# Optimization experiments

Measured on AMD Instinct MI355X. Metric: run time of the kernel, lower is better.

The kernel has to match this reference:

```python
import jax, jax.numpy as jnp
import numpy as np

N_NODES = 100000
N_EDGES = 1600000
D = 128
EPS = 0.0  # train_eps=False -> constant


def setup_inputs() -> dict:
    key = jax.random.key(0)
    k = jax.random.split(key, 6)
    s = 1.0 / np.sqrt(D)
    return {
        "X": jax.random.normal(k[0], (N_NODES, D), dtype=jnp.float32),
        "W1": jax.random.normal(k[1], (D, D), dtype=jnp.float32) * s,
        "b1": jnp.zeros((D,), dtype=jnp.float32),
        "W2": jax.random.normal(k[2], (D, D), dtype=jnp.float32) * s,
        "b2": jnp.zeros((D,), dtype=jnp.float32),
        "edge_src": jax.random.randint(k[3], (N_EDGES,), 0, N_NODES, dtype=jnp.int32),
        "edge_dst": jax.random.randint(k[4], (N_EDGES,), 0, N_NODES, dtype=jnp.int32),
    }


def reference(X, W1, b1, W2, b2, edge_src, edge_dst):
    # v2v sum aggregation: agg[i] = sum_{j in N(i)} X[j]
    msgs = X[edge_src]  # (E, D) gather
    agg = jax.ops.segment_sum(msgs, edge_dst, num_segments=N_NODES)  # (N, D)
    h = (1.0 + EPS) * X + agg
    # MLP: Linear -> ReLU -> Linear
    h = jax.nn.relu(h @ W1 + b1)
    out = h @ W2 + b2
    return out
```

## Files before the change

### kernel.cpp

```cpp
#include <hip/hip_runtime.h>
#include <hip/hip_bf16.h>

#define N_NODES 100000
#define N_EDGES 1600000
#define D 128

#define BINSHIFT 8
#define NB2 391
#define EPB 8192
#define RBLK 196
#define EBUF_CAP 4864

#define HEAD_W_BLOCKS 8
#define HEAD_CVT_BLOCKS 3125

#define PADK 136

typedef __bf16 bf16x8 __attribute__((ext_vector_type(8)));
typedef short short8 __attribute__((ext_vector_type(8)));
typedef float f32x4 __attribute__((ext_vector_type(4)));

__device__ __forceinline__ unsigned short f2bf(float f) {
  union { float f; unsigned u; } c; c.f = f;
  unsigned u = c.u;
  u += 0x7FFFu + ((u >> 16) & 1u);
  return (unsigned short)(u >> 16);
}
__device__ __forceinline__ float bflo(unsigned u) {
  union { unsigned u; float f; } c; c.u = u << 16; return c.f;
}
__device__ __forceinline__ float bfhi(unsigned u) {
  union { unsigned u; float f; } c; c.u = u & 0xFFFF0000u; return c.f;
}

__launch_bounds__(512)
__global__ void k_head(const int* __restrict__ esrc, const int* __restrict__ edst,
                       unsigned* __restrict__ binbuf, int* __restrict__ cntmatT,
                       int* __restrict__ startmatT,
                       const float* __restrict__ X, unsigned short* __restrict__ Xb,
                       const float* __restrict__ W1, const float* __restrict__ W2,
                       unsigned short* __restrict__ Wimg) {
  const int b = blockIdx.x, t = threadIdx.x;

  if (b < RBLK) {
    __shared__ unsigned lbuf[EPB];
    __shared__ int cnt[NB2];
    __shared__ int base[NB2];
    __shared__ int cur[NB2];
    __shared__ int scanb[512];
    const int e0 = b * EPB;
    const int ne = min(EPB, N_EDGES - e0);

    for (int i = t; i < NB2; i += 512) { cnt[i] = 0; cur[i] = 0; }
    __syncthreads();
    for (int i = t; i < ne; i += 512)
      atomicAdd(&cnt[edst[e0 + i] >> BINSHIFT], 1);
    __syncthreads();
    scanb[t] = (t < NB2) ? cnt[t] : 0;
    __syncthreads();
    for (int d = 1; d < 512; d <<= 1) {
      int x = (t >= d) ? scanb[t - d] : 0;
      __syncthreads();
      scanb[t] += x;
      __syncthreads();
    }
    if (t < NB2) base[t] = scanb[t] - cnt[t];
    __syncthreads();
    for (int i = t; i < ne; i += 512) {
      int d = edst[e0 + i];
      int s = esrc[e0 + i];
      int bi = d >> BINSHIFT;
      int pos = base[bi] + atomicAdd(&cur[bi], 1);
      lbuf[pos] = ((unsigned)(d & 255) << 17) | (unsigned)s;
    }
    __syncthreads();
    uint4* dst4 = (uint4*)(binbuf + (size_t)b * EPB);
    const uint4* src4 = (const uint4*)lbuf;
    for (int i = t; i < EPB / 4; i += 512) dst4[i] = src4[i];
    if (t < NB2) {
      cntmatT[t * RBLK + b] = cnt[t];
      startmatT[t * RBLK + b] = base[t];
    }
    return;
  }
  if (b < RBLK + HEAD_W_BLOCKS) {
    int bb = b - RBLK;
    const float* W = (bb & 4) ? W2 : W1;
    unsigned short* img = Wimg + ((bb & 4) ? 128 * PADK : 0);
    int k0 = (bb & 3) * 32;
#pragma unroll
    for (int it = 0; it < 8; ++it) {
      int idx = it * 512 + t;
      int k = k0 + (idx >> 7), n = idx & 127;
      img[n * PADK + k] = f2bf(W[k * 128 + n]);
    }
    return;
  }
  size_t i = ((size_t)(b - RBLK - HEAD_W_BLOCKS) * 512 + t) * 8;
  const float4* p = (const float4*)(X + i);
  float4 a = p[0], c = p[1];
  short8 s;
  s[0] = f2bf(a.x); s[1] = f2bf(a.y); s[2] = f2bf(a.z); s[3] = f2bf(a.w);
  s[4] = f2bf(c.x); s[5] = f2bf(c.y); s[6] = f2bf(c.z); s[7] = f2bf(c.w);
  *(short8*)(Xb + i) = s;
}

__launch_bounds__(1024)
__global__ void k_sortgather(const unsigned* __restrict__ binbuf,
                             const int* __restrict__ cntmatT,
                             const int* __restrict__ startmatT,
                             const unsigned* __restrict__ X1,
                             unsigned* __restrict__ h0) {
  __shared__ unsigned ebuf[EBUF_CAP];
  __shared__ unsigned ebuf2[EBUF_CAP];
  __shared__ int hist[256];
  __shared__ int scn[256];
  __shared__ int nstart[256];
  __shared__ int ncnt[256];
  __shared__ int rcnt[RBLK];
  __shared__ int roff[RBLK];
  __shared__ int eoff[RBLK];
  __shared__ int s_total;

  const int b = blockIdx.x, t = threadIdx.x;
  const int n0 = b << BINSHIFT;
  const int wv = t >> 6, ln = t & 63;

  if (t < RBLK) {
    rcnt[t] = cntmatT[b * RBLK + t];
    roff[t] = startmatT[b * RBLK + t];
  }
  __syncthreads();

  if (t < 256) scn[t] = (t < RBLK) ? rcnt[t] : 0;
  __syncthreads();
  for (int d = 1; d < 256; d <<= 1) {
    int x = 0;
    if (t < 256 && t >= d) x = scn[t - d];
    __syncthreads();
    if (t < 256) scn[t] += x;
    __syncthreads();
  }
  if (t < RBLK) eoff[t] = scn[t] - rcnt[t];
  if (t == RBLK - 1) s_total = scn[t];
  __syncthreads();
  const int mytotal = s_total;

  for (int r = wv; r < RBLK; r += 16) {
    const unsigned* src = binbuf + (size_t)r * EPB + roff[r];
    int c = rcnt[r], o = eoff[r];
    for (int i = ln; i < c; i += 64) ebuf[o + i] = src[i];
  }
  if (t < 256) hist[t] = 0;
  __syncthreads();

  for (int i = t; i < mytotal; i += 1024)
    atomicAdd(&hist[ebuf[i] >> 17], 1);
  __syncthreads();
  int v = (t < 256) ? hist[t] : 0;
  if (t < 256) scn[t] = v;
  __syncthreads();
  for (int d = 1; d < 256; d <<= 1) {
    int x = 0;
    if (t < 256 && t >= d) x = scn[t - d];
    __syncthreads();
    if (t < 256) scn[t] += x;
    __syncthreads();
  }
  if (t < 256) {
    nstart[t] = scn[t] - v;
    ncnt[t] = v;
    hist[t] = scn[t] - v;
  }
  __syncthreads();
  for (int i = t; i < mytotal; i += 1024) {
    unsigned e = ebuf[i];
    int pos = atomicAdd(&hist[e >> 17], 1);
    ebuf2[pos] = e & 0x1FFFFu;
  }
  __syncthreads();

  for (int j = 0; j < 16; ++j) {
    int li = wv * 16 + j;
    int node = n0 + li;
    if (node >= N_NODES) break;
    unsigned u = X1[(size_t)node * 64 + ln];
    float hx = bflo(u), hy = bfhi(u);
    int e = nstart[li];
    int end = e + ncnt[li];
    for (; e + 8 <= end; e += 8) {
      int s0 = ebuf2[e],     s1 = ebuf2[e + 1], s2 = ebuf2[e + 2], s3 = ebuf2[e + 3];
      int s4 = ebuf2[e + 4], s5 = ebuf2[e + 5], s6 = ebuf2[e + 6], s7 = ebuf2[e + 7];
      unsigned u0 = X1[(size_t)s0 * 64 + ln];
      unsigned u1 = X1[(size_t)s1 * 64 + ln];
      unsigned u2 = X1[(size_t)s2 * 64 + ln];
      unsigned u3 = X1[(size_t)s3 * 64 + ln];
      unsigned u4 = X1[(size_t)s4 * 64 + ln];
      unsigned u5 = X1[(size_t)s5 * 64 + ln];
      unsigned u6 = X1[(size_t)s6 * 64 + ln];
      unsigned u7 = X1[(size_t)s7 * 64 + ln];
      hx += bflo(u0); hy += bfhi(u0);
      hx += bflo(u1); hy += bfhi(u1);
      hx += bflo(u2); hy += bfhi(u2);
      hx += bflo(u3); hy += bfhi(u3);
      hx += bflo(u4); hy += bfhi(u4);
      hx += bflo(u5); hy += bfhi(u5);
      hx += bflo(u6); hy += bfhi(u6);
      hx += bflo(u7); hy += bfhi(u7);
    }
    for (; e + 2 <= end; e += 2) {
      unsigned u0 = X1[(size_t)ebuf2[e] * 64 + ln];
      unsigned u1 = X1[(size_t)ebuf2[e + 1] * 64 + ln];
      hx += bflo(u0); hy += bfhi(u0);
      hx += bflo(u1); hy += bfhi(u1);
    }
    for (; e < end; ++e) {
      unsigned u0 = X1[(size_t)ebuf2[e] * 64 + ln];
      hx += bflo(u0); hy += bfhi(u0);
    }
    h0[(size_t)node * 64 + ln] = ((unsigned)f2bf(hy) << 16) | f2bf(hx);
  }
}

#define BR2 128

__launch_bounds__(512, 4)
__global__ void k_mlp2(const unsigned short* __restrict__ h0,
                       const unsigned short* __restrict__ Wimg,
                       const float* __restrict__ b1v, const float* __restrict__ b2v,
                       float* __restrict__ out) {
  __shared__ __attribute__((aligned(16))) unsigned short lW[128 * PADK];
  __shared__ __attribute__((aligned(16))) unsigned short lH[BR2 * PADK];

  const int t = threadIdx.x;
  const int wave = t >> 6, lane = t & 63;
  const int lr = lane & 15, lg = lane >> 4;
  const int row0 = blockIdx.x * BR2;
  const int wrow = row0 + wave * 16;

  const uint4* wi = (const uint4*)Wimg;
  uint4* lw = (uint4*)lW;

  for (int i = t; i < 2176; i += 512) lw[i] = wi[i];

  bf16x8 a[4];
#pragma unroll
  for (int kb = 0; kb < 4; ++kb) {
    int r = wrow + lr;
    if (r >= N_NODES) r = N_NODES - 1;
    a[kb] = __builtin_bit_cast(bf16x8,
        *(const short8*)(h0 + (size_t)r * D + kb * 32 + lg * 8));
  }

  f32x4 acc[8];
#pragma unroll
  for (int nc = 0; nc < 8; ++nc) {
    float bb = b1v[nc * 16 + lr];
    acc[nc] = (f32x4){bb, bb, bb, bb};
  }

  __syncthreads();

#pragma unroll
  for (int nc = 0; nc < 8; ++nc) {
#pragma unroll
    for (int kb = 0; kb < 4; ++kb) {
      bf16x8 b = *(const bf16x8*)&lW[(nc * 16 + lr) * PADK + kb * 32 + lg * 8];
      acc[nc] = __builtin_amdgcn_mfma_f32_16x16x32_bf16(a[kb], b, acc[nc], 0, 0, 0);
    }
  }

  __syncthreads();

  {
    const uint4* wi2 = (const uint4*)Wimg + 2176;
    for (int i = t; i < 2176; i += 512) lw[i] = wi2[i];
  }

#pragma unroll
  for (int nc = 0; nc < 8; ++nc) {
#pragma unroll
    for (int r = 0; r < 4; ++r) {
      float v = acc[nc][r];
      v = v > 0.f ? v : 0.f;
      lH[(wave * 16 + lg * 4 + r) * PADK + nc * 16 + lr] = f2bf(v);
    }
  }

  __syncthreads();

  bf16x8 a2[4];
#pragma unroll
  for (int kb = 0; kb < 4; ++kb)
    a2[kb] = *(const bf16x8*)&lH[(wave * 16 + lr) * PADK + kb * 32 + lg * 8];

#pragma unroll
  for (int nc = 0; nc < 8; ++nc) {
    float bb = b2v[nc * 16 + lr];
    acc[nc] = (f32x4){bb, bb, bb, bb};
  }

#pragma unroll
  for (int nc = 0; nc < 8; ++nc) {
#pragma unroll
    for (int kb = 0; kb < 4; ++kb) {
      bf16x8 b = *(const bf16x8*)&lW[(nc * 16 + lr) * PADK + kb * 32 + lg * 8];
      acc[nc] = __builtin_amdgcn_mfma_f32_16x16x32_bf16(a2[kb], b, acc[nc], 0, 0, 0);
    }
  }

#pragma unroll
  for (int nc = 0; nc < 8; ++nc) {
#pragma unroll
    for (int r = 0; r < 4; ++r) {
      int row = wrow + lg * 4 + r;
      if (row < N_NODES) out[(size_t)row * D + nc * 16 + lr] = acc[nc][r];
    }
  }
}


__global__ void k_hist(const int* __restrict__ dst, int* __restrict__ deg) {
  int i = blockIdx.x * 256 + threadIdx.x;
  if (i < N_EDGES) atomicAdd(&deg[dst[i]], 1);
}

__global__ void k_scan1(const int* __restrict__ deg, int* __restrict__ offs,
                        int* __restrict__ bsum) {
  __shared__ int s[1024];
  int t = threadIdx.x;
  int i = blockIdx.x * 1024 + t;
  int v = (i < N_NODES) ? deg[i] : 0;
  s[t] = v;
  __syncthreads();
  for (int d = 1; d < 1024; d <<= 1) {
    int x = (t >= d) ? s[t - d] : 0;
    __syncthreads();
    s[t] += x;
    __syncthreads();
  }
  if (i < N_NODES) offs[i] = s[t] - v;
  if (t == 1023) bsum[blockIdx.x] = s[t];
}

__global__ void k_scan2(int* __restrict__ bsum) {
  __shared__ int s[128];
  int t = threadIdx.x;
  int v = (t < 98) ? bsum[t] : 0;
  s[t] = v;
  __syncthreads();
  for (int d = 1; d < 128; d <<= 1) {
    int x = (t >= d) ? s[t - d] : 0;
    __syncthreads();
    s[t] += x;
    __syncthreads();
  }
  if (t < 98) bsum[t] = s[t] - v;
}

__global__ void k_scan3(int* __restrict__ offs, const int* __restrict__ bsum) {
  int i = blockIdx.x * 1024 + threadIdx.x;
  if (i < N_NODES) offs[i] += bsum[blockIdx.x];
}

__global__ void k_bucket(const int* __restrict__ src, const int* __restrict__ dst,
                         int* __restrict__ offs, int* __restrict__ srt) {
  int i = blockIdx.x * 256 + threadIdx.x;
  if (i < N_EDGES) {
    int pos = atomicAdd(&offs[dst[i]], 1);
    srt[pos] = src[i];
  }
}

__global__ void k_gather(const float* __restrict__ X, const int* __restrict__ deg,
                         const int* __restrict__ offs, const int* __restrict__ srt,
                         float* __restrict__ out) {
  int node = blockIdx.x * 4 + (threadIdx.x >> 6);
  int lane = threadIdx.x & 63;
  const float2* X2 = (const float2*)X;
  float2 h = X2[(size_t)node * 64 + lane];
  int end = offs[node];
  int dg = deg[node];
  for (int e = end - dg; e < end; ++e) {
    int s = srt[e];
    float2 x = X2[(size_t)s * 64 + lane];
    h.x += x.x; h.y += x.y;
  }
  ((float2*)out)[(size_t)node * 64 + lane] = h;
}

#define BR 256

__launch_bounds__(512, 1)
__global__ void k_mlp(const float* __restrict__ h0,
                      const float* __restrict__ W1, const float* __restrict__ b1,
                      const float* __restrict__ W2, const float* __restrict__ b2,
                      float* __restrict__ out) {
  __shared__ __attribute__((aligned(16))) unsigned short lW[2 * 128 * PADK];
  __shared__ __attribute__((aligned(16))) unsigned short lH[BR * PADK];

  const int t = threadIdx.x;
  const int wave = t >> 6, lane = t & 63;
  const int lr = lane & 15, lg = lane >> 4;
  const int row0 = blockIdx.x * BR;
  const int wrow = row0 + wave * 32;

  for (int i = t; i < 128 * 128; i += 512) {
    int k = i >> 7, n = i & 127;
    lW[n * PADK + k] = f2bf(W1[i]);
    lW[128 * PADK + n * PADK + k] = f2bf(W2[i]);
  }

  bf16x8 a[2][4];
#pragma unroll
  for (int tr = 0; tr < 2; ++tr) {
#pragma unroll
    for (int kb = 0; kb < 4; ++kb) {
      int r = wrow + tr * 16 + lr;
      if (r >= N_NODES) r = N_NODES - 1;
      const float4* p = (const float4*)(h0 + (size_t)r * D + kb * 32 + lg * 8);
      float4 f0 = p[0], f1 = p[1];
      short8 s;
      s[0] = f2bf(f0.x); s[1] = f2bf(f0.y); s[2] = f2bf(f0.z); s[3] = f2bf(f0.w);
      s[4] = f2bf(f1.x); s[5] = f2bf(f1.y); s[6] = f2bf(f1.z); s[7] = f2bf(f1.w);
      a[tr][kb] = __builtin_bit_cast(bf16x8, s);
    }
  }

  f32x4 acc[2][8];
#pragma unroll
  for (int nc = 0; nc < 8; ++nc) {
    float bb = b1[nc * 16 + lr];
#pragma unroll
    for (int tr = 0; tr < 2; ++tr) acc[tr][nc] = (f32x4){bb, bb, bb, bb};
  }

  __syncthreads();

#pragma unroll
  for (int nc = 0; nc < 8; ++nc) {
#pragma unroll
    for (int kb = 0; kb < 4; ++kb) {
      bf16x8 b = *(const bf16x8*)&lW[(nc * 16 + lr) * PADK + kb * 32 + lg * 8];
#pragma unroll
      for (int tr = 0; tr < 2; ++tr)
        acc[tr][nc] = __builtin_amdgcn_mfma_f32_16x16x32_bf16(a[tr][kb], b, acc[tr][nc], 0, 0, 0);
    }
  }

#pragma unroll
  for (int tr = 0; tr < 2; ++tr) {
#pragma unroll
    for (int nc = 0; nc < 8; ++nc) {
#pragma unroll
      for (int r = 0; r < 4; ++r) {
        float v = acc[tr][nc][r];
        v = v > 0.f ? v : 0.f;
        int lrow = wave * 32 + tr * 16 + lg * 4 + r;
        lH[lrow * PADK + nc * 16 + lr] = f2bf(v);
      }
    }
  }

  __syncthreads();

  bf16x8 a2[2][4];
#pragma unroll
  for (int tr = 0; tr < 2; ++tr) {
#pragma unroll
    for (int kb = 0; kb < 4; ++kb)
      a2[tr][kb] = *(const bf16x8*)&lH[(wave * 32 + tr * 16 + lr) * PADK + kb * 32 + lg * 8];
  }

#pragma unroll
  for (int nc = 0; nc < 8; ++nc) {
    float bb = b2[nc * 16 + lr];
#pragma unroll
    for (int tr = 0; tr < 2; ++tr) acc[tr][nc] = (f32x4){bb, bb, bb, bb};
  }

#pragma unroll
  for (int nc = 0; nc < 8; ++nc) {
#pragma unroll
    for (int kb = 0; kb < 4; ++kb) {
      bf16x8 b = *(const bf16x8*)&lW[128 * PADK + (nc * 16 + lr) * PADK + kb * 32 + lg * 8];
#pragma unroll
      for (int tr = 0; tr < 2; ++tr)
        acc[tr][nc] = __builtin_amdgcn_mfma_f32_16x16x32_bf16(a2[tr][kb], b, acc[tr][nc], 0, 0, 0);
    }
  }

#pragma unroll
  for (int tr = 0; tr < 2; ++tr) {
#pragma unroll
    for (int nc = 0; nc < 8; ++nc) {
#pragma unroll
      for (int r = 0; r < 4; ++r) {
        int row = wrow + tr * 16 + lg * 4 + r;
        if (row < N_NODES) out[(size_t)row * D + nc * 16 + lr] = acc[tr][nc][r];
      }
    }
  }
}

extern "C" void kernel_launch(void* const* d_in, const int* in_sizes, int n_in,
                              void* d_out, int out_size, void* d_ws, size_t ws_size,
                              hipStream_t stream) {
  const float* X  = (const float*)d_in[0];
  const float* W1 = (const float*)d_in[1];
  const float* b1 = (const float*)d_in[2];
  const float* W2 = (const float*)d_in[3];
  const float* b2 = (const float*)d_in[4];
  const int* esrc = (const int*)d_in[5];
  const int* edst = (const int*)d_in[6];
  float* out = (float*)d_out;

  char* ws = (char*)d_ws;
  unsigned* binbuf = (unsigned*)(ws);
  int* cntmatT   = (int*)(ws + 6422528);
  int* startmatT = (int*)(ws + 6729088);
  unsigned short* Xb  = (unsigned short*)(ws + 7035648);
  unsigned short* h0b = (unsigned short*)(ws + 32635648);
  unsigned short* Wimg = (unsigned short*)(ws + 58235648);
  const size_t NEED = 58305280;

  if (ws_size >= NEED) {
    k_head<<<RBLK + HEAD_W_BLOCKS + HEAD_CVT_BLOCKS, 512, 0, stream>>>(
        esrc, edst, binbuf, cntmatT, startmatT, X, Xb, W1, W2, Wimg);
    k_sortgather<<<NB2, 1024, 0, stream>>>(binbuf, cntmatT, startmatT,
                                           (const unsigned*)Xb, (unsigned*)h0b);
    k_mlp2<<<(N_NODES + BR2 - 1) / BR2, 512, 0, stream>>>(h0b, Wimg, b1, b2, out);
  } else {
    int* deg  = (int*)(ws);
    int* offs = (int*)(ws + 400000);
    int* bsum = (int*)(ws + 800000);
    int* srtF = (int*)(ws + 802048);
    hipMemsetAsync(deg, 0, N_NODES * sizeof(int), stream);
    k_hist  <<<N_EDGES / 256, 256, 0, stream>>>(edst, deg);
    k_scan1 <<<98, 1024, 0, stream>>>(deg, offs, bsum);
    k_scan2 <<<1, 128, 0, stream>>>(bsum);
    k_scan3 <<<98, 1024, 0, stream>>>(offs, bsum);
    k_bucket<<<N_EDGES / 256, 256, 0, stream>>>(esrc, edst, offs, srtF);
    k_gather<<<N_NODES / 4, 256, 0, stream>>>(X, deg, offs, srtF, out);
    k_mlp   <<<(N_NODES + BR - 1) / BR, 512, 0, stream>>>(out, W1, b1, W2, b2, out);
  }
}
```

Baseline: 118.6 us.

## Halve node bins to 128 nodes, pack count/offset matrix, rebalance block sizes

Changes binning from 256 to 128 destination nodes per bin, which doubles the number of sort-gather blocks (782) and runs each with 512 threads and smaller LDS buffers, so more blocks fit per CU and the work is spread more evenly. The head kernel now uses 1024 threads per block, and the separate count and start matrices are packed into one 32-bit word each, reducing metadata traffic. Costs include more bins to scan in the head kernel and more per-block overhead in the sort-gather kernel. The 16-bit packing depends on counts and offsets staying below 65536, which holds for EPB of 8192.

Measured after the change: 143.4 us. 21.0% more time.

```diff
diff --git a/kernel.cpp b/kernel.cpp
--- a/kernel.cpp
+++ b/kernel.cpp
@@ -5,14 +5,14 @@
 #define N_EDGES 1600000
 #define D 128
 
-#define BINSHIFT 8
-#define NB2 391
+#define BINSHIFT 7
+#define NB2 782
 #define EPB 8192
 #define RBLK 196
-#define EBUF_CAP 4864
-
-#define HEAD_W_BLOCKS 8
-#define HEAD_CVT_BLOCKS 3125
+#define EBUF_CAP 2688
+
+#define HEAD_W_BLOCKS 4
+#define HEAD_CVT_BLOCKS 1563
 
 #define PADK 136
 
@@ -33,10 +33,9 @@
   union { unsigned u; float f; } c; c.u = u & 0xFFFF0000u; return c.f;
 }
 
-__launch_bounds__(512)
+__launch_bounds__(1024)
 __global__ void k_head(const int* __restrict__ esrc, const int* __restrict__ edst,
-                       unsigned* __restrict__ binbuf, int* __restrict__ cntmatT,
-                       int* __restrict__ startmatT,
+                       unsigned* __restrict__ binbuf, unsigned* __restrict__ matT,
                        const float* __restrict__ X, unsigned short* __restrict__ Xb,
                        const float* __restrict__ W1, const float* __restrict__ W2,
                        unsigned short* __restrict__ Wimg) {
@@ -47,18 +46,18 @@
     __shared__ int cnt[NB2];
     __shared__ int base[NB2];
     __shared__ int cur[NB2];
-    __shared__ int scanb[512];
+    __shared__ int scanb[1024];
     const int e0 = b * EPB;
     const int ne = min(EPB, N_EDGES - e0);
 
-    for (int i = t; i < NB2; i += 512) { cnt[i] = 0; cur[i] = 0; }
-    __syncthreads();
-    for (int i = t; i < ne; i += 512)
+    if (t < NB2) { cnt[t] = 0; cur[t] = 0; }
+    __syncthreads();
+    for (int i = t; i < ne; i += 1024)
       atomicAdd(&cnt[edst[e0 + i] >> BINSHIFT], 1);
     __syncthreads();
     scanb[t] = (t < NB2) ? cnt[t] : 0;
     __syncthreads();
-    for (int d = 1; d < 512; d <<= 1) {
+    for (int d = 1; d < 1024; d <<= 1) {
       int x = (t >= d) ? scanb[t - d] : 0;
       __syncthreads();
       scanb[t] += x;
@@ -66,37 +65,35 @@
     }
     if (t < NB2) base[t] = scanb[t] - cnt[t];
     __syncthreads();
-    for (int i = t; i < ne; i += 512) {
+    for (int i = t; i < ne; i += 1024) {
       int d = edst[e0 + i];
       int s = esrc[e0 + i];
       int bi = d >> BINSHIFT;
       int pos = base[bi] + atomicAdd(&cur[bi], 1);
-      lbuf[pos] = ((unsigned)(d & 255) << 17) | (unsigned)s;
+      lbuf[pos] = ((unsigned)(d & 127) << 17) | (unsigned)s;
     }
     __syncthreads();
     uint4* dst4 = (uint4*)(binbuf + (size_t)b * EPB);
     const uint4* src4 = (const uint4*)lbuf;
-    for (int i = t; i < EPB / 4; i += 512) dst4[i] = src4[i];
-    if (t < NB2) {
-      cntmatT[t * RBLK + b] = cnt[t];
-      startmatT[t * RBLK + b] = base[t];
-    }
+    for (int i = t; i < EPB / 4; i += 1024) dst4[i] = src4[i];
+    if (t < NB2)
+      matT[t * RBLK + b] = ((unsigned)base[t] << 16) | (unsigned)cnt[t];
     return;
   }
   if (b < RBLK + HEAD_W_BLOCKS) {
     int bb = b - RBLK;
-    const float* W = (bb & 4) ? W2 : W1;
-    unsigned short* img = Wimg + ((bb & 4) ? 128 * PADK : 0);
-    int k0 = (bb & 3) * 32;
 #pragma unroll
     for (int it = 0; it < 8; ++it) {
-      int idx = it * 512 + t;
-      int k = k0 + (idx >> 7), n = idx & 127;
-      img[n * PADK + k] = f2bf(W[k * 128 + n]);
+      int widx = bb * 8192 + it * 1024 + t;
+      int fi = widx & 16383;
+      const float* W = (widx >> 14) ? W2 : W1;
+      int k = fi >> 7, n = fi & 127;
+      Wimg[(widx >> 14) * 128 * PADK + n * PADK + k] = f2bf(W[k * 128 + n]);
     }
     return;
   }
-  size_t i = ((size_t)(b - RBLK - HEAD_W_BLOCKS) * 512 + t) * 8;
+  size_t i = ((size_t)(b - RBLK - HEAD_W_BLOCKS) * 1024 + t) * 8;
+  if (i >= (size_t)N_NODES * D) return;
   const float4* p = (const float4*)(X + i);
   float4 a = p[0], c = p[1];
   short8 s;
@@ -105,18 +102,17 @@
   *(short8*)(Xb + i) = s;
 }
 
-__launch_bounds__(1024)
+__launch_bounds__(512)
 __global__ void k_sortgather(const unsigned* __restrict__ binbuf,
-                             const int* __restrict__ cntmatT,
-                             const int* __restrict__ startmatT,
+                             const unsigned* __restrict__ matT,
                              const unsigned* __restrict__ X1,
                              unsigned* __restrict__ h0) {
   __shared__ unsigned ebuf[EBUF_CAP];
   __shared__ unsigned ebuf2[EBUF_CAP];
-  __shared__ int hist[256];
+  __shared__ int hist[128];
   __shared__ int scn[256];
-  __shared__ int nstart[256];
-  __shared__ int ncnt[256];
+  __shared__ int nstart[128];
+  __shared__ int ncnt[128];
   __shared__ int rcnt[RBLK];
   __shared__ int roff[RBLK];
   __shared__ int eoff[RBLK];
@@ -127,8 +123,9 @@
   const int wv = t >> 6, ln = t & 63;
 
   if (t < RBLK) {
-    rcnt[t] = cntmatT[b * RBLK + t];
-    roff[t] = startmatT[b * RBLK + t];
+    unsigned m = matT[b * RBLK + t];
+    rcnt[t] = (int)(m & 0xFFFFu);
+    roff[t] = (int)(m >> 16);
   }
   __syncthreads();
 
@@ -146,34 +143,34 @@
   __syncthreads();
   const int mytotal = s_total;
 
-  for (int r = wv; r < RBLK; r += 16) {
+  for (int r = wv; r < RBLK; r += 8) {
     const unsigned* src = binbuf + (size_t)r * EPB + roff[r];
     int c = rcnt[r], o = eoff[r];
     for (int i = ln; i < c; i += 64) ebuf[o + i] = src[i];
   }
-  if (t < 256) hist[t] = 0;
-  __syncthreads();
-
-  for (int i = t; i < mytotal; i += 1024)
+  if (t < 128) hist[t] = 0;
+  __syncthreads();
+
+  for (int i = t; i < mytotal; i += 512)
     atomicAdd(&hist[ebuf[i] >> 17], 1);
   __syncthreads();
-  int v = (t < 256) ? hist[t] : 0;
-  if (t < 256) scn[t] = v;
-  __syncthreads();
-  for (int d = 1; d < 256; d <<= 1) {
+  int v = (t < 128) ? hist[t] : 0;
+  if (t < 128) scn[t] = v;
+  __syncthreads();
+  for (int d = 1; d < 128; d <<= 1) {
     int x = 0;
-    if (t < 256 && t >= d) x = scn[t - d];
-    __syncthreads();
-    if (t < 256) scn[t] += x;
-    __syncthreads();
-  }
-  if (t < 256) {
+    if (t < 128 && t >= d) x = scn[t - d];
+    __syncthreads();
+    if (t < 128) scn[t] += x;
+    __syncthreads();
+  }
+  if (t < 128) {
     nstart[t] = scn[t] - v;
     ncnt[t] = v;
     hist[t] = scn[t] - v;
   }
   __syncthreads();
-  for (int i = t; i < mytotal; i += 1024) {
+  for (int i = t; i < mytotal; i += 512) {
     unsigned e = ebuf[i];
     int pos = atomicAdd(&hist[e >> 17], 1);
     ebuf2[pos] = e & 0x1FFFFu;
@@ -517,18 +514,17 @@
 
   char* ws = (char*)d_ws;
   unsigned* binbuf = (unsigned*)(ws);
-  int* cntmatT   = (int*)(ws + 6422528);
-  int* startmatT = (int*)(ws + 6729088);
-  unsigned short* Xb  = (unsigned short*)(ws + 7035648);
-  unsigned short* h0b = (unsigned short*)(ws + 32635648);
-  unsigned short* Wimg = (unsigned short*)(ws + 58235648);
-  const size_t NEED = 58305280;
+  unsigned* matT   = (unsigned*)(ws + 6422528);
+  unsigned short* Xb  = (unsigned short*)(ws + 7035616);
+  unsigned short* h0b = (unsigned short*)(ws + 32635616);
+  unsigned short* Wimg = (unsigned short*)(ws + 58235616);
+  const size_t NEED = 58305248;
 
   if (ws_size >= NEED) {
-    k_head<<<RBLK + HEAD_W_BLOCKS + HEAD_CVT_BLOCKS, 512, 0, stream>>>(
-        esrc, edst, binbuf, cntmatT, startmatT, X, Xb, W1, W2, Wimg);
-    k_sortgather<<<NB2, 1024, 0, stream>>>(binbuf, cntmatT, startmatT,
-                                           (const unsigned*)Xb, (unsigned*)h0b);
+    k_head<<<RBLK + HEAD_W_BLOCKS + HEAD_CVT_BLOCKS, 1024, 0, stream>>>(
+        esrc, edst, binbuf, matT, X, Xb, W1, W2, Wimg);
+    k_sortgather<<<NB2, 512, 0, stream>>>(binbuf, matT,
+                                          (const unsigned*)Xb, (unsigned*)h0b);
     k_mlp2<<<(N_NODES + BR2 - 1) / BR2, 512, 0, stream>>>(h0b, Wimg, b1, b2, out);
   } else {
     int* deg  = (int*)(ws);
```
